# Kernel optimization log

Measured on AMD Instinct MI355X. Metric: run time of the kernel, lower is better.

The kernel has to match this reference:

```python
import jax, jax.numpy as jnp
import numpy as np

# kernel hyperparameters (base_params)
NUGGET = 0.001
REG_LAMBDA = 0.01
FIT_L, FIT_SIGMA = 1.0, 1.0
MMD_L, MMD_SIGMA = 1.0, 1.0
N, D = 4096, 4


def rbf_gram(X1, X2, l, sigma):
    # [N1,N2] radial kernel: sigma^2 * exp(-||x-x'||^2 / (2 l^2)), vectorized
    sq = (jnp.sum(X1 * X1, axis=1)[:, None]
          + jnp.sum(X2 * X2, axis=1)[None, :]
          - 2.0 * (X1 @ X2.T))
    sq = jnp.maximum(sq, 0.0)
    return (sigma * sigma) * jnp.exp(-sq / (2.0 * l * l))


def setup_inputs() -> dict:
    key = jax.random.key(0)
    kx, ky, kz = jax.random.split(key, 3)
    X = jax.random.normal(kx, (N, D), dtype=jnp.float32)
    Y = jax.random.normal(ky, (N, D), dtype=jnp.float32)
    Z = Y + 0.1 * jax.random.normal(kz, (N, D), dtype=jnp.float32)  # Z init'd from Y, perturbed
    return {"X": X, "Y": Y, "Z": Z}


def reference(X, Y, Z):
    # fit_kXX and its nugget-regularized inverse (precomputed in __init__)
    fit_kXX = rbf_gram(X, X, FIT_L, FIT_SIGMA)
    fit_kXX_inv = jnp.linalg.inv(fit_kXX + NUGGET * jnp.eye(X.shape[0], dtype=X.dtype))

    # loss_fit_z: ||k_ZZ||_F^2 - 2 ||k_ZY||_F^2  (torch matrix norm = Frobenius)
    k_ZZ = rbf_gram(Z, Z, MMD_L, MMD_SIGMA)
    k_ZY = rbf_gram(Z, Y, MMD_L, MMD_SIGMA)
    loss_fit = jnp.sum(k_ZZ * k_ZZ) - 2.0 * jnp.sum(k_ZY * k_ZY)

    # loss_reg_z: reg_lambda * trace(Z^T fit_kXX_inv Z)
    loss_reg = REG_LAMBDA * jnp.sum(Z * (fit_kXX_inv @ Z))

    return loss_fit + loss_reg
```

## Files before the change

### kernel.cpp

```cpp
#include <hip/hip_runtime.h>


#define NN   4096
#define LDA  4100
#define OFF_W ((size_t)NN*LDA)
#define OFF_ACC_B ((OFF_W + (size_t)NN*4)*4)

__device__ __forceinline__ float rdlane(float v, int l){
    return __int_as_float(__builtin_amdgcn_readlane(__float_as_int(v), l));
}

__global__ void k_build_A(const float* __restrict__ X, float* __restrict__ A){
    const int i  = blockIdx.y;
    const int j0 = (blockIdx.x*256 + threadIdx.x)*4;
    const float4 xi = *(const float4*)(X + (size_t)i*4);
    float out[4];
#pragma unroll
    for (int s=0;s<4;s++){
        const float4 xj = *(const float4*)(X + (size_t)(j0+s)*4);
        float d0=xi.x-xj.x, d1=xi.y-xj.y, d2=xi.z-xj.z, d3=xi.w-xj.w;
        float sq = d0*d0+d1*d1+d2*d2+d3*d3;
        float v  = __expf(-0.5f*sq);
        if (i == j0+s) v += 0.001f;
        out[s]=v;
    }
    *(float4*)(A + (size_t)i*LDA + j0) = make_float4(out[0],out[1],out[2],out[3]);
}

__device__ void wave_chol64(const float* Dm, float* __restrict__ A, int k2){
    const int lane = threadIdx.x & 63;
    float row[64];
#pragma unroll
    for (int q=0;q<16;q++){
        float4 v = *(const float4*)(Dm + lane*68 + q*4);
        row[q*4]=v.x; row[q*4+1]=v.y; row[q*4+2]=v.z; row[q*4+3]=v.w;
    }
#pragma unroll
    for (int j=0;j<64;j++){
        float d  = rdlane(row[j], j);
        float sd = sqrtf(d);
        float inv= 1.0f/sd;
        float v  = (lane==j)? sd : row[j]*inv;
        row[j] = v;
#pragma unroll
        for (int c=j+1;c<64;c++){
            float lc = rdlane(v, c);
            row[c] -= v*lc;
        }
    }
#pragma unroll
    for (int q=0;q<16;q++)
        *(float4*)(A + (size_t)(k2+lane)*LDA + k2 + q*4) =
            make_float4(row[q*4],row[q*4+1],row[q*4+2],row[q*4+3]);
}

__global__ __launch_bounds__(256) void k_step(float* __restrict__ A, float* __restrict__ W,
                                              const float* __restrict__ Z, int s){
    __shared__ float S[8704];
    const int tid = threadIdx.x;
    const int bid = blockIdx.x;
    const int k2   = (s+1)*64;
    const int T    = 63 - s;
    const int T2   = (T+1)>>1;
    const int nT2  = T2*(T2+1)/2;
    const int kcol = s*64;

    if (bid == 0){
        float* P  = S;
        float* Dm = S + 4352;
        if (s >= 0){
#pragma unroll
            for (int it=0; it<4; ++it){
                int idx = tid + it*256;
                int r = idx>>4, q = idx&15;
                float4 v = *(const float4*)(A + (size_t)(k2+r)*LDA + kcol + q*4);
                P[(q*4+0)*68+r]=v.x; P[(q*4+1)*68+r]=v.y;
                P[(q*4+2)*68+r]=v.z; P[(q*4+3)*68+r]=v.w;
            }
            __syncthreads();
            const int tx = tid&15, ty = tid>>4;
            float acc[4][4]={};
#pragma unroll 8
            for (int t=0;t<64;t++){
                float4 a = *(const float4*)&P[t*68 + ty*4];
                float4 b = *(const float4*)&P[t*68 + tx*4];
                acc[0][0]+=a.x*b.x; acc[0][1]+=a.x*b.y; acc[0][2]+=a.x*b.z; acc[0][3]+=a.x*b.w;
                acc[1][0]+=a.y*b.x; acc[1][1]+=a.y*b.y; acc[1][2]+=a.y*b.z; acc[1][3]+=a.y*b.w;
                acc[2][0]+=a.z*b.x; acc[2][1]+=a.z*b.y; acc[2][2]+=a.z*b.z; acc[2][3]+=a.z*b.w;
                acc[3][0]+=a.w*b.x; acc[3][1]+=a.w*b.y; acc[3][2]+=a.w*b.z; acc[3][3]+=a.w*b.w;
            }
#pragma unroll
            for (int i=0;i<4;i++){
                float4 c = *(const float4*)(A + (size_t)(k2+ty*4+i)*LDA + k2 + tx*4);
                c.x-=acc[i][0]; c.y-=acc[i][1]; c.z-=acc[i][2]; c.w-=acc[i][3];
                *(float4*)&Dm[(ty*4+i)*68 + tx*4] = c;
            }
        } else {
#pragma unroll
            for (int it=0; it<4; ++it){
                int idx = tid + it*256;
                int r = idx>>4, q = idx&15;
                float4 v = *(const float4*)(A + (size_t)(k2+r)*LDA + k2 + q*4);
                *(float4*)&Dm[r*68 + q*4] = v;
            }
        }
        __syncthreads();
        if (tid < 64) wave_chol64(Dm, A, k2);
    } else if (bid <= nT2){
        int t2 = bid-1;
        int bi = (int)((sqrtf(8.f*(float)t2+1.f)-1.f)*0.5f);
        while ((bi+1)*(bi+2)/2 <= t2) ++bi;
        while (bi*(bi+1)/2 > t2) --bi;
        const int bj = t2 - bi*(bi+1)/2;
        const int r0 = k2 + bi*128, c0 = k2 + bj*128;
        const int diag = (bi==bj);
        float* Sa = S;
        float* Sb = diag ? S : (S + 4224);
        const int tx = tid&15, ty = tid>>4;
        float acc[8][8]={};
        for (int kk=0; kk<2; ++kk){
            const int kb = kcol + kk*32;
#pragma unroll
            for (int it=0; it<4; ++it){
                int idx = tid + it*256;
                int row = idx>>3, q = idx&7;
                int rl = r0+row; if (rl>4095) rl=4095;
                float4 v = *(const float4*)(A + (size_t)rl*LDA + kb + q*4);
                Sa[(q*4+0)*132+row]=v.x; Sa[(q*4+1)*132+row]=v.y;
                Sa[(q*4+2)*132+row]=v.z; Sa[(q*4+3)*132+row]=v.w;
            }
            if (!diag){
#pragma unroll
                for (int it=0; it<4; ++it){
                    int idx = tid + it*256;
                    int row = idx>>3, q = idx&7;
                    int cl = c0+row; if (cl>4095) cl=4095;
                    float4 v = *(const float4*)(A + (size_t)cl*LDA + kb + q*4);
                    Sb[(q*4+0)*132+row]=v.x; Sb[(q*4+1)*132+row]=v.y;
                    Sb[(q*4+2)*132+row]=v.z; Sb[(q*4+3)*132+row]=v.w;
                }
            }
            __syncthreads();
#pragma unroll 4
            for (int t=0;t<32;t++){
                float4 a0 = *(const float4*)&Sa[t*132 + ty*8];
                float4 a1 = *(const float4*)&Sa[t*132 + ty*8 + 4];
                float4 b0 = *(const float4*)&Sb[t*132 + tx*8];
                float4 b1 = *(const float4*)&Sb[t*132 + tx*8 + 4];
                float av[8]={a0.x,a0.y,a0.z,a0.w,a1.x,a1.y,a1.z,a1.w};
                float bv[8]={b0.x,b0.y,b0.z,b0.w,b1.x,b1.y,b1.z,b1.w};
#pragma unroll
                for (int i=0;i<8;i++)
#pragma unroll
                    for (int j=0;j<8;j++) acc[i][j] += av[i]*bv[j];
            }
            __syncthreads();
        }
#pragma unroll
        for (int i=0;i<8;i++){
            const int r = r0 + ty*8 + i;
            if (r > 4095) continue;
#pragma unroll
            for (int jq=0;jq<2;jq++){
                const int c = c0 + tx*8 + jq*4;
                if (c > 4095) continue;
                if (r < k2+64 && c < k2+64) continue;
                float* p = A + (size_t)r*LDA + c;
                float4 cv = *(float4*)p;
                cv.x -= acc[i][jq*4+0]; cv.y -= acc[i][jq*4+1];
                cv.z -= acc[i][jq*4+2]; cv.w -= acc[i][jq*4+3];
                *(float4*)p = cv;
            }
        }
    } else {
        const int wu = bid - 1 - nT2;
        const int rrow = k2 + wu*64;
        float* Lt = S;
        float* Ws = S + 4352;
#pragma unroll
        for (int it=0; it<4; ++it){
            int idx = tid + it*256;
            int r = idx>>4, q = idx&15;
            float4 v = *(const float4*)(A + (size_t)(rrow+r)*LDA + kcol + q*4);
            *(float4*)&Lt[r*68 + q*4] = v;
        }
        if (tid < 64){
            float4 v = *(const float4*)(W + (size_t)(kcol+tid)*4);
            *(float4*)&Ws[tid*4] = v;
        }
        __syncthreads();
        if (tid < 64){
            const float* wsrc = (s==0) ? (Z + (size_t)(rrow+tid)*4) : (W + (size_t)(rrow+tid)*4);
            float4 w = *(const float4*)wsrc;
#pragma unroll 8
            for (int t=0;t<64;t++){
                float l = Lt[tid*68 + t];
                float4 x = *(const float4*)&Ws[t*4];
                w.x -= l*x.x; w.y -= l*x.y; w.z -= l*x.z; w.w -= l*x.w;
            }
            *(float4*)(W + (size_t)(rrow+tid)*4) = w;
        }
    }
}

__global__ __launch_bounds__(256) void k_trsm2(float* __restrict__ A, float* __restrict__ W,
                                               const float* __restrict__ Z, int s){
    __shared__ float Ld[64*68];
    __shared__ float dinv[64];
    const int tid = threadIdx.x;
    const int s0  = s*64;
#pragma unroll
    for (int it=0; it<4; ++it){
        int idx = tid + it*256;
        int r = idx>>4, q = idx&15;
        float4 v = *(const float4*)(A + (size_t)(s0+r)*LDA + s0 + q*4);
        *(float4*)&Ld[r*68 + q*4] = v;
    }
    __syncthreads();
    if (tid < 64) dinv[tid] = 1.0f/Ld[tid*68 + tid];
    __syncthreads();

    const int nRB = (63-s+3)>>2;
    if ((int)blockIdx.x < nRB){
        const int row = s0 + 64 + blockIdx.x*256 + tid;
        const int rl  = row>4095 ? 4095 : row;
        float x[64];
        const float* src = A + (size_t)rl*LDA + s0;
#pragma unroll
        for (int q=0;q<16;q++){
            float4 v = *(const float4*)(src + q*4);
            x[q*4]=v.x; x[q*4+1]=v.y; x[q*4+2]=v.z; x[q*4+3]=v.w;
        }
#pragma unroll
        for (int c=0;c<64;c++){
            float xc = x[c]*dinv[c];
            x[c] = xc;
#pragma unroll
            for (int t=c+1;t<64;t++) x[t] -= xc*Ld[t*68 + c];
        }
        if (row < 4096){
            float* dst = A + (size_t)row*LDA + s0;
#pragma unroll
            for (int q=0;q<16;q++)
                *(float4*)(dst + q*4) = make_float4(x[q*4],x[q*4+1],x[q*4+2],x[q*4+3]);
        }
    } else {
        if (tid < 64){
            const int lane = tid;
            const float* wsrc = (s==0) ? (Z + (size_t)(s0+lane)*4) : (W + (size_t)(s0+lane)*4);
            float4 wv = *(const float4*)wsrc;
            float w0=wv.x, w1=wv.y, w2=wv.z, w3=wv.w;
#pragma unroll
            for (int j=0;j<64;j++){
                if (lane==j){ float dj=dinv[j]; w0*=dj; w1*=dj; w2*=dj; w3*=dj; }
                float b0=__shfl(w0,j), b1=__shfl(w1,j), b2=__shfl(w2,j), b3=__shfl(w3,j);
                float l = Ld[lane*68 + j];
                if (lane>j){ w0-=l*b0; w1-=l*b1; w2-=l*b2; w3-=l*b3; }
            }
            *(float4*)(W + (size_t)(s0+lane)*4) = make_float4(w0,w1,w2,w3);
        }
    }
}

__global__ void k_lossfit(const float* __restrict__ Z, const float* __restrict__ Y,
                          double* __restrict__ acc){
    const int tid=threadIdx.x;
    const int i0=blockIdx.x*8;
    double s=0.0;
    for (int ii=0;ii<8;ii++){
        const float4 zi = *(const float4*)(Z + (size_t)(i0+ii)*4);
        for (int j=tid;j<NN;j+=256){
            float4 zj = *(const float4*)(Z + (size_t)j*4);
            float4 yj = *(const float4*)(Y + (size_t)j*4);
            float d0=zi.x-zj.x, d1=zi.y-zj.y, d2=zi.z-zj.z, d3=zi.w-zj.w;
            float dzz = d0*d0+d1*d1+d2*d2+d3*d3;
            d0=zi.x-yj.x; d1=zi.y-yj.y; d2=zi.z-yj.z; d3=zi.w-yj.w;
            float dzy = d0*d0+d1*d1+d2*d2+d3*d3;
            s += (double)(__expf(-dzz) - 2.f*__expf(-dzy));
        }
    }
    for (int o=32;o;o>>=1) s += __shfl_down(s,o);
    __shared__ double ps[4];
    if ((tid&63)==0) ps[tid>>6]=s;
    __syncthreads();
    if (tid==0) atomicAdd(acc, ps[0]+ps[1]+ps[2]+ps[3]);
}

__global__ void k_zero(double* acc){ if (threadIdx.x==0) acc[0]=0.0; }

__global__ void k_finish(const float* __restrict__ W, const double* __restrict__ acc,
                         float* __restrict__ out){
    const int tid=threadIdx.x;
    double s=0.0;
    for (int r=tid;r<NN;r+=256){
        float4 v=*(const float4*)(W+(size_t)r*4);
        s += (double)v.x*v.x+(double)v.y*v.y+(double)v.z*v.z+(double)v.w*v.w;
    }
    for (int o=32;o;o>>=1) s += __shfl_down(s,o);
    __shared__ double ps[4];
    if ((tid&63)==0) ps[tid>>6]=s;
    __syncthreads();
    if (tid==0) out[0] = (float)(acc[0] + 0.01*(ps[0]+ps[1]+ps[2]+ps[3]));
}

extern "C" void kernel_launch(void* const* d_in, const int* in_sizes, int n_in,
                              void* d_out, int out_size, void* d_ws, size_t ws_size,
                              hipStream_t stream){
    const float* X=(const float*)d_in[0];
    const float* Y=(const float*)d_in[1];
    const float* Z=(const float*)d_in[2];
    float* ws   = (float*)d_ws;
    float* A    = ws;
    float* W    = ws + OFF_W;
    double* acc = (double*)((char*)d_ws + OFF_ACC_B);

    if (ws_size < OFF_ACC_B + 64) return;

    k_zero   <<<1,64,0,stream>>>(acc);
    k_lossfit<<<512,256,0,stream>>>(Z,Y,acc);
    k_build_A<<<dim3(NN/1024,NN),256,0,stream>>>(X,A);

    k_step<<<1,256,0,stream>>>(A,W,Z,-1);
    for (int s=0;s<64;s++){
        const int T = 63-s;
        const int nRB = (T+3)>>2;
        k_trsm2<<<nRB+1,256,0,stream>>>(A,W,Z,s);
        if (s < 63){
            const int T2 = (T+1)>>1;
            const int nT2 = T2*(T2+1)/2;
            k_step<<<nT2+1+T,256,0,stream>>>(A,W,Z,s);
        }
    }
    k_finish<<<1,256,0,stream>>>(W,acc,(float*)d_out);
}
```

Baseline: 3.492 ms.

## Restructure Cholesky into 256-wide panels with flag-synchronized intra-panel blocks

Replaces the 64-column right-looking Cholesky (about 127 launches) with 16 super-steps. Each step runs one panel kernel whose blocks factor four 64-column diagonal blocks, compute explicit inverses of the diagonal blocks, and apply them by GEMM instead of TRSM. Blocks coordinate through global atomic flags with spin waits. Each step is followed by a single rank-256 trailing update that register-prefetches its tiles. The aim is to cut kernel-launch count and serial TRSM latency, at the cost of spin-wait deadlock risk if the panel blocks are not co-resident, and extra inversion error.

Result: no change. 3.477 ms (-0.4%).

```diff
diff --git a/kernel.cpp b/kernel.cpp
--- a/kernel.cpp
+++ b/kernel.cpp
@@ -1,13 +1,28 @@
 #include <hip/hip_runtime.h>
 
 
-#define NN   4096
-#define LDA  4100
-#define OFF_W ((size_t)NN*LDA)
-#define OFF_ACC_B ((OFF_W + (size_t)NN*4)*4)
+#define NN 4096
+#define LDA 4100
+#define OFF_W     ((size_t)NN*LDA)
+#define OFF_LINV  (OFF_W + (size_t)NN*4)
+#define OFF_FLAGS (OFF_LINV + (size_t)4*4096)
+#define OFF_ACC   (OFF_FLAGS + 512)
+
+#define FD(S,i)   ((S)*4+(i))
+#define FH(S,i,c) (64 + ((S)*4+(i))*4 + (c))
 
 __device__ __forceinline__ float rdlane(float v, int l){
     return __int_as_float(__builtin_amdgcn_readlane(__float_as_int(v), l));
+}
+__device__ __forceinline__ void spin_flag(int* f, int idx){
+    while (__hip_atomic_load(&f[idx], __ATOMIC_RELAXED, __HIP_MEMORY_SCOPE_AGENT) == 0)
+        __builtin_amdgcn_s_sleep(8);
+    __builtin_amdgcn_fence(__ATOMIC_ACQUIRE, "agent");
+}
+__device__ __forceinline__ void pub_flag(int* f, int idx){
+    __syncthreads();
+    if (threadIdx.x == 0)
+        __hip_atomic_store(&f[idx], 1, __ATOMIC_RELEASE, __HIP_MEMORY_SCOPE_AGENT);
 }
 
 __global__ void k_build_A(const float* __restrict__ X, float* __restrict__ A){
@@ -27,238 +42,275 @@
     *(float4*)(A + (size_t)i*LDA + j0) = make_float4(out[0],out[1],out[2],out[3]);
 }
 
-__device__ void wave_chol64(const float* Dm, float* __restrict__ A, int k2){
-    const int lane = threadIdx.x & 63;
-    float row[64];
-#pragma unroll
-    for (int q=0;q<16;q++){
-        float4 v = *(const float4*)(Dm + lane*68 + q*4);
-        row[q*4]=v.x; row[q*4+1]=v.y; row[q*4+2]=v.z; row[q*4+3]=v.w;
-    }
-#pragma unroll
-    for (int j=0;j<64;j++){
-        float d  = rdlane(row[j], j);
-        float sd = sqrtf(d);
-        float inv= 1.0f/sd;
-        float v  = (lane==j)? sd : row[j]*inv;
-        row[j] = v;
-#pragma unroll
-        for (int c=j+1;c<64;c++){
-            float lc = rdlane(v, c);
-            row[c] -= v*lc;
-        }
-    }
-#pragma unroll
-    for (int q=0;q<16;q++)
-        *(float4*)(A + (size_t)(k2+lane)*LDA + k2 + q*4) =
-            make_float4(row[q*4],row[q*4+1],row[q*4+2],row[q*4+3]);
-}
-
-__global__ __launch_bounds__(256) void k_step(float* __restrict__ A, float* __restrict__ W,
-                                              const float* __restrict__ Z, int s){
-    __shared__ float S[8704];
+__global__ __launch_bounds__(256) void k_panel(float* __restrict__ A, float* __restrict__ W,
+                                               float* __restrict__ LinvTg, int* __restrict__ flags,
+                                               int S){
+    __shared__ float Po[64*68];
+    __shared__ float LiT[64*68];
+    __shared__ float LnT[64*68];
+    __shared__ float Wi[64*4];
+    __shared__ float Mt[16*17];
     const int tid = threadIdx.x;
-    const int bid = blockIdx.x;
-    const int k2   = (s+1)*64;
-    const int T    = 63 - s;
-    const int T2   = (T+1)>>1;
-    const int nT2  = T2*(T2+1)/2;
-    const int kcol = s*64;
-
-    if (bid == 0){
-        float* P  = S;
-        float* Dm = S + 4352;
-        if (s >= 0){
-#pragma unroll
-            for (int it=0; it<4; ++it){
-                int idx = tid + it*256;
-                int r = idx>>4, q = idx&15;
-                float4 v = *(const float4*)(A + (size_t)(k2+r)*LDA + kcol + q*4);
-                P[(q*4+0)*68+r]=v.x; P[(q*4+1)*68+r]=v.y;
-                P[(q*4+2)*68+r]=v.z; P[(q*4+3)*68+r]=v.w;
-            }
-            __syncthreads();
-            const int tx = tid&15, ty = tid>>4;
-            float acc[4][4]={};
+    const int j   = blockIdx.x;
+    const int k0  = S*256;
+    const int r0  = k0 + j*64;
+    const int tx = tid&15, ty = tid>>4;
+    const bool head = (j < 4);
+    const int nsteps = head ? j : 4;
+
+    for (int i=0; i<nsteps; ++i){
+        const int ci = k0 + i*64;
+        spin_flag(flags, FD(S,i));
+        __syncthreads();
+#pragma unroll
+        for (int it=0; it<4; ++it){
+            int idx = tid + it*256, r = idx>>4, q = idx&15;
+            float4 v = *(const float4*)(A + (size_t)(r0+r)*LDA + ci + q*4);
+            Po[(q*4+0)*68+r]=v.x; Po[(q*4+1)*68+r]=v.y;
+            Po[(q*4+2)*68+r]=v.z; Po[(q*4+3)*68+r]=v.w;
+            float4 u = *(const float4*)(LinvTg + (size_t)i*4096 + (size_t)idx*4);
+            int t = idx>>4, c4 = (idx&15)*4;
+            *(float4*)&LiT[t*68 + c4] = u;
+        }
+        if (tid < 64) *(float4*)&Wi[tid*4] = *(const float4*)(W + (size_t)(k0+i*64+tid)*4);
+        __syncthreads();
+        float acc[4][4]={};
+#pragma unroll 8
+        for (int t=0;t<64;t++){
+            float4 a = *(const float4*)&Po[t*68 + ty*4];
+            float4 b = *(const float4*)&LiT[t*68 + tx*4];
+            acc[0][0]+=a.x*b.x; acc[0][1]+=a.x*b.y; acc[0][2]+=a.x*b.z; acc[0][3]+=a.x*b.w;
+            acc[1][0]+=a.y*b.x; acc[1][1]+=a.y*b.y; acc[1][2]+=a.y*b.z; acc[1][3]+=a.y*b.w;
+            acc[2][0]+=a.z*b.x; acc[2][1]+=a.z*b.y; acc[2][2]+=a.z*b.z; acc[2][3]+=a.z*b.w;
+            acc[3][0]+=a.w*b.x; acc[3][1]+=a.w*b.y; acc[3][2]+=a.w*b.z; acc[3][3]+=a.w*b.w;
+        }
+#pragma unroll
+        for (int ii=0;ii<4;ii++)
+            *(float4*)(A + (size_t)(r0+ty*4+ii)*LDA + ci + tx*4) =
+                make_float4(acc[ii][0],acc[ii][1],acc[ii][2],acc[ii][3]);
+#pragma unroll
+        for (int ii=0;ii<4;ii++)
+#pragma unroll
+            for (int jj=0;jj<4;jj++)
+                LnT[(tx*4+jj)*68 + ty*4+ii] = acc[ii][jj];
+        if (head) pub_flag(flags, FH(S,i,j));
+        else __syncthreads();
+        const int c2max = head ? j : 3;
+        for (int c2=i+1; c2<=c2max; ++c2){
+            const float* Bsrc;
+            if (c2 != j){
+                spin_flag(flags, FH(S,i,c2));
+                __syncthreads();
+#pragma unroll
+                for (int it=0; it<4; ++it){
+                    int idx = tid + it*256, r = idx>>4, q = idx&15;
+                    float4 v = *(const float4*)(A + (size_t)(k0+c2*64+r)*LDA + ci + q*4);
+                    LiT[(q*4+0)*68+r]=v.x; LiT[(q*4+1)*68+r]=v.y;
+                    LiT[(q*4+2)*68+r]=v.z; LiT[(q*4+3)*68+r]=v.w;
+                }
+                __syncthreads();
+                Bsrc = LiT;
+            } else {
+                Bsrc = LnT;
+            }
+            float ua[4][4]={};
 #pragma unroll 8
             for (int t=0;t<64;t++){
-                float4 a = *(const float4*)&P[t*68 + ty*4];
-                float4 b = *(const float4*)&P[t*68 + tx*4];
-                acc[0][0]+=a.x*b.x; acc[0][1]+=a.x*b.y; acc[0][2]+=a.x*b.z; acc[0][3]+=a.x*b.w;
-                acc[1][0]+=a.y*b.x; acc[1][1]+=a.y*b.y; acc[1][2]+=a.y*b.z; acc[1][3]+=a.y*b.w;
-                acc[2][0]+=a.z*b.x; acc[2][1]+=a.z*b.y; acc[2][2]+=a.z*b.z; acc[2][3]+=a.z*b.w;
-                acc[3][0]+=a.w*b.x; acc[3][1]+=a.w*b.y; acc[3][2]+=a.w*b.z; acc[3][3]+=a.w*b.w;
-            }
-#pragma unroll
-            for (int i=0;i<4;i++){
-                float4 c = *(const float4*)(A + (size_t)(k2+ty*4+i)*LDA + k2 + tx*4);
-                c.x-=acc[i][0]; c.y-=acc[i][1]; c.z-=acc[i][2]; c.w-=acc[i][3];
-                *(float4*)&Dm[(ty*4+i)*68 + tx*4] = c;
-            }
-        } else {
-#pragma unroll
-            for (int it=0; it<4; ++it){
-                int idx = tid + it*256;
-                int r = idx>>4, q = idx&15;
-                float4 v = *(const float4*)(A + (size_t)(k2+r)*LDA + k2 + q*4);
-                *(float4*)&Dm[r*68 + q*4] = v;
-            }
-        }
-        __syncthreads();
-        if (tid < 64) wave_chol64(Dm, A, k2);
-    } else if (bid <= nT2){
-        int t2 = bid-1;
-        int bi = (int)((sqrtf(8.f*(float)t2+1.f)-1.f)*0.5f);
-        while ((bi+1)*(bi+2)/2 <= t2) ++bi;
-        while (bi*(bi+1)/2 > t2) --bi;
-        const int bj = t2 - bi*(bi+1)/2;
-        const int r0 = k2 + bi*128, c0 = k2 + bj*128;
-        const int diag = (bi==bj);
-        float* Sa = S;
-        float* Sb = diag ? S : (S + 4224);
-        const int tx = tid&15, ty = tid>>4;
-        float acc[8][8]={};
-        for (int kk=0; kk<2; ++kk){
-            const int kb = kcol + kk*32;
-#pragma unroll
-            for (int it=0; it<4; ++it){
-                int idx = tid + it*256;
-                int row = idx>>3, q = idx&7;
-                int rl = r0+row; if (rl>4095) rl=4095;
-                float4 v = *(const float4*)(A + (size_t)rl*LDA + kb + q*4);
-                Sa[(q*4+0)*132+row]=v.x; Sa[(q*4+1)*132+row]=v.y;
-                Sa[(q*4+2)*132+row]=v.z; Sa[(q*4+3)*132+row]=v.w;
-            }
-            if (!diag){
-#pragma unroll
-                for (int it=0; it<4; ++it){
-                    int idx = tid + it*256;
-                    int row = idx>>3, q = idx&7;
-                    int cl = c0+row; if (cl>4095) cl=4095;
-                    float4 v = *(const float4*)(A + (size_t)cl*LDA + kb + q*4);
-                    Sb[(q*4+0)*132+row]=v.x; Sb[(q*4+1)*132+row]=v.y;
-                    Sb[(q*4+2)*132+row]=v.z; Sb[(q*4+3)*132+row]=v.w;
-                }
-            }
-            __syncthreads();
-#pragma unroll 4
-            for (int t=0;t<32;t++){
-                float4 a0 = *(const float4*)&Sa[t*132 + ty*8];
-                float4 a1 = *(const float4*)&Sa[t*132 + ty*8 + 4];
-                float4 b0 = *(const float4*)&Sb[t*132 + tx*8];
-                float4 b1 = *(const float4*)&Sb[t*132 + tx*8 + 4];
-                float av[8]={a0.x,a0.y,a0.z,a0.w,a1.x,a1.y,a1.z,a1.w};
-                float bv[8]={b0.x,b0.y,b0.z,b0.w,b1.x,b1.y,b1.z,b1.w};
-#pragma unroll
-                for (int i=0;i<8;i++)
-#pragma unroll
-                    for (int j=0;j<8;j++) acc[i][j] += av[i]*bv[j];
-            }
-            __syncthreads();
-        }
-#pragma unroll
-        for (int i=0;i<8;i++){
-            const int r = r0 + ty*8 + i;
-            if (r > 4095) continue;
-#pragma unroll
-            for (int jq=0;jq<2;jq++){
-                const int c = c0 + tx*8 + jq*4;
-                if (c > 4095) continue;
-                if (r < k2+64 && c < k2+64) continue;
-                float* p = A + (size_t)r*LDA + c;
+                float4 a = *(const float4*)&LnT[t*68 + ty*4];
+                float4 b = *(const float4*)&Bsrc[t*68 + tx*4];
+                ua[0][0]+=a.x*b.x; ua[0][1]+=a.x*b.y; ua[0][2]+=a.x*b.z; ua[0][3]+=a.x*b.w;
+                ua[1][0]+=a.y*b.x; ua[1][1]+=a.y*b.y; ua[1][2]+=a.y*b.z; ua[1][3]+=a.y*b.w;
+                ua[2][0]+=a.z*b.x; ua[2][1]+=a.z*b.y; ua[2][2]+=a.z*b.z; ua[2][3]+=a.z*b.w;
+                ua[3][0]+=a.w*b.x; ua[3][1]+=a.w*b.y; ua[3][2]+=a.w*b.z; ua[3][3]+=a.w*b.w;
+            }
+#pragma unroll
+            for (int ii=0;ii<4;ii++){
+                float* p = A + (size_t)(r0+ty*4+ii)*LDA + k0+c2*64 + tx*4;
                 float4 cv = *(float4*)p;
-                cv.x -= acc[i][jq*4+0]; cv.y -= acc[i][jq*4+1];
-                cv.z -= acc[i][jq*4+2]; cv.w -= acc[i][jq*4+3];
+                cv.x-=ua[ii][0]; cv.y-=ua[ii][1]; cv.z-=ua[ii][2]; cv.w-=ua[ii][3];
                 *(float4*)p = cv;
             }
         }
-    } else {
-        const int wu = bid - 1 - nT2;
-        const int rrow = k2 + wu*64;
-        float* Lt = S;
-        float* Ws = S + 4352;
+        {
+            int row = tid>>2, cw = tid&3;
+            float s = 0.f;
+#pragma unroll 16
+            for (int t=0;t<64;t++) s += LnT[t*68+row]*Wi[t*4+cw];
+            float* wp = W + (size_t)(r0+row)*4 + cw;
+            *wp = *wp - s;
+        }
+        __syncthreads();
+    }
+
+    if (head){
+        const int ci = k0 + j*64;
+        __syncthreads();
 #pragma unroll
         for (int it=0; it<4; ++it){
-            int idx = tid + it*256;
-            int r = idx>>4, q = idx&15;
-            float4 v = *(const float4*)(A + (size_t)(rrow+r)*LDA + kcol + q*4);
-            *(float4*)&Lt[r*68 + q*4] = v;
-        }
-        if (tid < 64){
-            float4 v = *(const float4*)(W + (size_t)(kcol+tid)*4);
-            *(float4*)&Ws[tid*4] = v;
-        }
-        __syncthreads();
-        if (tid < 64){
-            const float* wsrc = (s==0) ? (Z + (size_t)(rrow+tid)*4) : (W + (size_t)(rrow+tid)*4);
-            float4 w = *(const float4*)wsrc;
-#pragma unroll 8
-            for (int t=0;t<64;t++){
-                float l = Lt[tid*68 + t];
-                float4 x = *(const float4*)&Ws[t*4];
-                w.x -= l*x.x; w.y -= l*x.y; w.z -= l*x.z; w.w -= l*x.w;
-            }
-            *(float4*)(W + (size_t)(rrow+tid)*4) = w;
-        }
-    }
-}
-
-__global__ __launch_bounds__(256) void k_trsm2(float* __restrict__ A, float* __restrict__ W,
-                                               const float* __restrict__ Z, int s){
-    __shared__ float Ld[64*68];
-    __shared__ float dinv[64];
-    const int tid = threadIdx.x;
-    const int s0  = s*64;
-#pragma unroll
-    for (int it=0; it<4; ++it){
-        int idx = tid + it*256;
-        int r = idx>>4, q = idx&15;
-        float4 v = *(const float4*)(A + (size_t)(s0+r)*LDA + s0 + q*4);
-        *(float4*)&Ld[r*68 + q*4] = v;
-    }
-    __syncthreads();
-    if (tid < 64) dinv[tid] = 1.0f/Ld[tid*68 + tid];
-    __syncthreads();
-
-    const int nRB = (63-s+3)>>2;
-    if ((int)blockIdx.x < nRB){
-        const int row = s0 + 64 + blockIdx.x*256 + tid;
-        const int rl  = row>4095 ? 4095 : row;
-        float x[64];
-        const float* src = A + (size_t)rl*LDA + s0;
-#pragma unroll
-        for (int q=0;q<16;q++){
-            float4 v = *(const float4*)(src + q*4);
-            x[q*4]=v.x; x[q*4+1]=v.y; x[q*4+2]=v.z; x[q*4+3]=v.w;
-        }
-#pragma unroll
-        for (int c=0;c<64;c++){
-            float xc = x[c]*dinv[c];
-            x[c] = xc;
-#pragma unroll
-            for (int t=c+1;t<64;t++) x[t] -= xc*Ld[t*68 + c];
-        }
-        if (row < 4096){
-            float* dst = A + (size_t)row*LDA + s0;
-#pragma unroll
-            for (int q=0;q<16;q++)
-                *(float4*)(dst + q*4) = make_float4(x[q*4],x[q*4+1],x[q*4+2],x[q*4+3]);
-        }
-    } else {
+            int idx = tid + it*256, r = idx>>4, q = idx&15;
+            float4 v = *(const float4*)(A + (size_t)(r0+r)*LDA + ci + q*4);
+            *(float4*)&Po[r*68 + q*4] = v;
+        }
+        __syncthreads();
+        float row[64];
         if (tid < 64){
             const int lane = tid;
-            const float* wsrc = (s==0) ? (Z + (size_t)(s0+lane)*4) : (W + (size_t)(s0+lane)*4);
-            float4 wv = *(const float4*)wsrc;
-            float w0=wv.x, w1=wv.y, w2=wv.z, w3=wv.w;
-#pragma unroll
-            for (int j=0;j<64;j++){
-                if (lane==j){ float dj=dinv[j]; w0*=dj; w1*=dj; w2*=dj; w3*=dj; }
-                float b0=__shfl(w0,j), b1=__shfl(w1,j), b2=__shfl(w2,j), b3=__shfl(w3,j);
-                float l = Ld[lane*68 + j];
-                if (lane>j){ w0-=l*b0; w1-=l*b1; w2-=l*b2; w3-=l*b3; }
-            }
-            *(float4*)(W + (size_t)(s0+lane)*4) = make_float4(w0,w1,w2,w3);
-        }
+#pragma unroll
+            for (int q=0;q<16;q++){
+                float4 v = *(const float4*)&Po[lane*68 + q*4];
+                row[q*4]=v.x; row[q*4+1]=v.y; row[q*4+2]=v.z; row[q*4+3]=v.w;
+            }
+#pragma unroll
+            for (int jj=0;jj<64;jj++){
+                float d  = rdlane(row[jj], jj);
+                float sd = sqrtf(d);
+                float inv= 1.0f/sd;
+                float v  = (lane==jj)? sd : row[jj]*inv;
+                row[jj] = v;
+#pragma unroll
+                for (int c=jj+1;c<64;c++){
+                    float lc = rdlane(v, c);
+                    row[c] -= v*lc;
+                }
+            }
+#pragma unroll
+            for (int q=0;q<16;q++){
+                float4 v = make_float4(row[q*4],row[q*4+1],row[q*4+2],row[q*4+3]);
+                *(float4*)(A + (size_t)(r0+lane)*LDA + ci + q*4) = v;
+                *(float4*)&Po[lane*68 + q*4] = v;
+            }
+        }
+        __syncthreads();
+        for (int idx=tid; idx<4096; idx+=256){
+            int r = idx>>6, c = idx&63;
+            if (r < c) LiT[r*68+c] = 0.f;
+        }
+        __syncthreads();
+        {
+            const int d = tid>>6, cc = (tid>>2)&15, g = tid&3;
+            const int c = d*16 + cc, hi = (d+1)*16;
+            for (int jj=c; jj<hi; ++jj){
+                float part = 0.f;
+                for (int t=c+g; t<jj; t+=4) part += Po[jj*68+t]*LiT[t*68+c];
+                part += __shfl_xor(part,1);
+                part += __shfl_xor(part,2);
+                float x = ((jj==c)?1.f:0.f) - part;
+                x /= Po[jj*68+jj];
+                if (g==0) LiT[jj*68+c] = x;
+            }
+        }
+        __syncthreads();
+        {
+            const int r16 = tid>>4, c16 = tid&15;
+            for (int sdist=1; sdist<4; ++sdist){
+                for (int bc=0; bc+sdist<4; ++bc){
+                    const int br = bc + sdist;
+                    float m = 0.f;
+                    for (int k=bc; k<br; ++k)
+#pragma unroll 4
+                        for (int t2=0;t2<16;t2++)
+                            m += Po[(16*br+r16)*68 + 16*k+t2] * LiT[(16*k+t2)*68 + 16*bc+c16];
+                    Mt[r16*17+c16] = m;
+                    __syncthreads();
+                    float x = 0.f;
+#pragma unroll 4
+                    for (int t=0;t<16;t++)
+                        x += LiT[(16*br+r16)*68 + 16*br+t] * Mt[t*17+c16];
+                    __syncthreads();
+                    LiT[(16*br+r16)*68 + 16*bc+c16] = -x;
+                    __syncthreads();
+                }
+            }
+        }
+        for (int idx=tid; idx<4096; idx+=256){
+            int t = idx>>6, c = idx&63;
+            LinvTg[(size_t)j*4096 + idx] = LiT[c*68 + t];
+        }
+        if (tid < 64){
+            const int lane = tid;
+            float4 wv = *(const float4*)(W + (size_t)(r0+lane)*4);
+            float w0=wv.x,w1=wv.y,w2=wv.z,w3=wv.w;
+            const float myinv = 1.f/row[lane];
+#pragma unroll
+            for (int jj=0;jj<64;jj++){
+                if (lane==jj){ w0*=myinv; w1*=myinv; w2*=myinv; w3*=myinv; }
+                float b0=__shfl(w0,jj), b1=__shfl(w1,jj), b2=__shfl(w2,jj), b3=__shfl(w3,jj);
+                float l = row[jj];
+                if (lane>jj){ w0-=l*b0; w1-=l*b1; w2-=l*b2; w3-=l*b3; }
+            }
+            *(float4*)(W + (size_t)(r0+lane)*4) = make_float4(w0,w1,w2,w3);
+        }
+        pub_flag(flags, FD(S,j));
+    }
+}
+
+__global__ __launch_bounds__(256) void k_upd256(float* __restrict__ A, int S){
+    __shared__ float Sa[32*132];
+    __shared__ float Sb[32*132];
+    const int tid = threadIdx.x;
+    const int k0 = S*256, base = k0+256;
+    int t2 = blockIdx.x;
+    int bi = (int)((sqrtf(8.f*(float)t2+1.f)-1.f)*0.5f);
+    while ((bi+1)*(bi+2)/2 <= t2) ++bi;
+    while (bi*(bi+1)/2 > t2) --bi;
+    const int bj = t2 - bi*(bi+1)/2;
+    const int r0 = base + bi*128, c0 = base + bj*128;
+    const bool dg = (bi==bj);
+    const float* Sbp = dg ? Sa : Sb;
+    const int tx = tid&15, ty = tid>>4;
+    int row_[4], q_[4];
+#pragma unroll
+    for (int it=0;it<4;++it){ int idx=tid+it*256; row_[it]=idx>>3; q_[it]=idx&7; }
+    float4 ra[4], rb[4];
+#pragma unroll
+    for (int it=0;it<4;++it){
+        ra[it] = *(const float4*)(A + (size_t)(r0+row_[it])*LDA + k0 + q_[it]*4);
+        if (!dg) rb[it] = *(const float4*)(A + (size_t)(c0+row_[it])*LDA + k0 + q_[it]*4);
+    }
+    float acc[8][8]={};
+    for (int kk=0;kk<8;++kk){
+        __syncthreads();
+#pragma unroll
+        for (int it=0;it<4;++it){
+            Sa[(q_[it]*4+0)*132+row_[it]]=ra[it].x; Sa[(q_[it]*4+1)*132+row_[it]]=ra[it].y;
+            Sa[(q_[it]*4+2)*132+row_[it]]=ra[it].z; Sa[(q_[it]*4+3)*132+row_[it]]=ra[it].w;
+            if (!dg){
+                Sb[(q_[it]*4+0)*132+row_[it]]=rb[it].x; Sb[(q_[it]*4+1)*132+row_[it]]=rb[it].y;
+                Sb[(q_[it]*4+2)*132+row_[it]]=rb[it].z; Sb[(q_[it]*4+3)*132+row_[it]]=rb[it].w;
+            }
+        }
+        __syncthreads();
+        if (kk < 7){
+            const int kb = k0 + (kk+1)*32;
+#pragma unroll
+            for (int it=0;it<4;++it){
+                ra[it] = *(const float4*)(A + (size_t)(r0+row_[it])*LDA + kb + q_[it]*4);
+                if (!dg) rb[it] = *(const float4*)(A + (size_t)(c0+row_[it])*LDA + kb + q_[it]*4);
+            }
+        }
+#pragma unroll 4
+        for (int t=0;t<32;++t){
+            float4 a0 = *(const float4*)&Sa[t*132 + ty*8];
+            float4 a1 = *(const float4*)&Sa[t*132 + ty*8 + 4];
+            float4 b0 = *(const float4*)&Sbp[t*132 + tx*8];
+            float4 b1 = *(const float4*)&Sbp[t*132 + tx*8 + 4];
+            float av[8]={a0.x,a0.y,a0.z,a0.w,a1.x,a1.y,a1.z,a1.w};
+            float bv[8]={b0.x,b0.y,b0.z,b0.w,b1.x,b1.y,b1.z,b1.w};
+#pragma unroll
+            for (int i=0;i<8;i++)
+#pragma unroll
+                for (int jj=0;jj<8;jj++) acc[i][jj] += av[i]*bv[jj];
+        }
+    }
+#pragma unroll
+    for (int ii=0;ii<8;ii++){
+        float* p = A + (size_t)(r0+ty*8+ii)*LDA + c0 + tx*8;
+        float4 c1 = *(float4*)p;
+        c1.x-=acc[ii][0]; c1.y-=acc[ii][1]; c1.z-=acc[ii][2]; c1.w-=acc[ii][3];
+        *(float4*)p = c1;
+        float4 c2 = *(float4*)(p+4);
+        c2.x-=acc[ii][4]; c2.y-=acc[ii][5]; c2.z-=acc[ii][6]; c2.w-=acc[ii][7];
+        *(float4*)(p+4) = c2;
     }
 }
 
@@ -286,7 +338,15 @@
     if (tid==0) atomicAdd(acc, ps[0]+ps[1]+ps[2]+ps[3]);
 }
 
-__global__ void k_zero(double* acc){ if (threadIdx.x==0) acc[0]=0.0; }
+__global__ void k_zero(double* acc, int* flags){
+    if (threadIdx.x==0) acc[0]=0.0;
+    if (threadIdx.x<512) flags[threadIdx.x]=0;
+}
+
+__global__ void k_copyZ(const float* __restrict__ Z, float* __restrict__ W){
+    const int i = blockIdx.x*256+threadIdx.x;
+    ((float4*)W)[i] = ((const float4*)Z)[i];
+}
 
 __global__ void k_finish(const float* __restrict__ W, const double* __restrict__ acc,
                          float* __restrict__ out){
@@ -309,27 +369,28 @@
     const float* X=(const float*)d_in[0];
     const float* Y=(const float*)d_in[1];
     const float* Z=(const float*)d_in[2];
-    float* ws   = (float*)d_ws;
-    float* A    = ws;
-    float* W    = ws + OFF_W;
-    double* acc = (double*)((char*)d_ws + OFF_ACC_B);
-
-    if (ws_size < OFF_ACC_B + 64) return;
-
-    k_zero   <<<1,64,0,stream>>>(acc);
-    k_lossfit<<<512,256,0,stream>>>(Z,Y,acc);
-    k_build_A<<<dim3(NN/1024,NN),256,0,stream>>>(X,A);
-
-    k_step<<<1,256,0,stream>>>(A,W,Z,-1);
-    for (int s=0;s<64;s++){
-        const int T = 63-s;
-        const int nRB = (T+3)>>2;
-        k_trsm2<<<nRB+1,256,0,stream>>>(A,W,Z,s);
-        if (s < 63){
-            const int T2 = (T+1)>>1;
+    float* ws    = (float*)d_ws;
+    float* A     = ws;
+    float* W     = ws + OFF_W;
+    float* LinvT = ws + OFF_LINV;
+    int*   flags = (int*)(ws + OFF_FLAGS);
+    double* acc  = (double*)(ws + OFF_ACC);
+
+    if (ws_size < (OFF_ACC + 4)*sizeof(float) + 16) return;
+
+    k_zero   <<<1,512,0,stream>>>(acc, flags);
+    k_copyZ  <<<16,256,0,stream>>>(Z, W);
+    k_build_A<<<dim3(NN/1024,NN),256,0,stream>>>(X, A);
+    k_lossfit<<<512,256,0,stream>>>(Z, Y, acc);
+
+    for (int S=0; S<16; ++S){
+        const int nblk = 64 - 4*S;
+        k_panel<<<nblk,256,0,stream>>>(A, W, LinvT, flags, S);
+        if (S < 15){
+            const int T2 = 30 - 2*S;
             const int nT2 = T2*(T2+1)/2;
-            k_step<<<nT2+1+T,256,0,stream>>>(A,W,Z,s);
-        }
-    }
-    k_finish<<<1,256,0,stream>>>(W,acc,(float*)d_out);
-}
+            k_upd256<<<nT2,256,0,stream>>>(A, S);
+        }
+    }
+    k_finish<<<1,256,0,stream>>>(W, acc, (float*)d_out);
+}
```
